# Optimization experiments

Measured on AMD Instinct MI355X. Metric: run time of the kernel, lower is better.

The kernel has to match this reference:

```python
import jax, jax.numpy as jnp
import numpy as np

B, H, W, C = 4, 64, 64, 64


def _self_atten(x, q_w, q_b, v_w, v_b, dim):
    # x: [B, N, dim]; torch Linear weight is [out, in] -> x @ W.T + b
    q = jnp.einsum('bnd,od->bno', x, q_w) + q_b
    k = q  # original module uses q_linear for both q and k
    v = jnp.einsum('bnd,od->bno', x, v_w) + v_b
    a = jax.nn.sigmoid(jnp.einsum('bnd,bmd->bnm', q, k) / jnp.sqrt(jnp.float32(dim)))
    return jnp.einsum('bnm,bmd->bnd', a, v)


def setup_inputs() -> dict:
    key = jax.random.key(0)
    ks = jax.random.split(key, 11)
    s = 0.05
    return {
        'x': jax.random.normal(ks[0], (B, H, W, C), jnp.float32),
        'hq_w': jax.random.normal(ks[1], (H, H), jnp.float32) * s,
        'hq_b': jax.random.normal(ks[2], (H,), jnp.float32) * s,
        'hv_w': jax.random.normal(ks[3], (H, H), jnp.float32) * s,
        'hv_b': jax.random.normal(ks[4], (H,), jnp.float32) * s,
        'wq_w': jax.random.normal(ks[5], (W, W), jnp.float32) * s,
        'wq_b': jax.random.normal(ks[6], (W,), jnp.float32) * s,
        'wv_w': jax.random.normal(ks[7], (W, W), jnp.float32) * s,
        'wv_b': jax.random.normal(ks[8], (W,), jnp.float32) * s,
        'h_weight': jax.random.normal(ks[9], (1,), jnp.float32) * s,
        'w_weight': jax.random.normal(ks[10], (1,), jnp.float32) * s,
    }


def reference(x, hq_w, hq_b, hv_w, hv_b, wq_w, wq_b, wv_w, wv_b, h_weight, w_weight):
    b, h, w, c = x.shape
    # height axis attention: seq = W*C, feature dim = H
    xh = jnp.transpose(x, (0, 2, 3, 1)).reshape(b, w * c, h)
    xh = _self_atten(xh, hq_w, hq_b, hv_w, hv_b, h)
    xh = jnp.transpose(xh.reshape(b, w, c, h), (0, 3, 1, 2))  # [B,H,W,C]
    x = xh * h_weight + x
    # width axis attention: seq = H*C, feature dim = W
    xw = jnp.transpose(x, (0, 1, 3, 2)).reshape(b, h * c, w)
    xw = _self_atten(xw, wq_w, wq_b, wv_w, wv_b, w)
    xw = jnp.transpose(xw.reshape(b, h, c, w), (0, 1, 3, 2))  # [B,H,W,C]
    x = xw * w_weight + x
    return x
```

## Files before the change

kernel.cpp:

```cpp
#include <hip/hip_runtime.h>
#include <hip/hip_bf16.h>


typedef __attribute__((ext_vector_type(8)))  short        short8;
typedef __attribute__((ext_vector_type(16))) float        f32x16;
typedef __attribute__((ext_vector_type(4)))  unsigned int u32x4;
typedef __attribute__((ext_vector_type(2)))  unsigned int u32x2;
typedef __attribute__((ext_vector_type(4)))  float        f32x4;

#define BHWC (4096 * 64)
#define ALPHA 0.42466089f

__device__ __forceinline__ unsigned short f2bf(float f) {
    __hip_bfloat16 h = __float2bfloat16(f);
    union { __hip_bfloat16 h; unsigned short u; } c; c.h = h;
    return c.u;
}
__device__ __forceinline__ float sigfast(float x) {
    float e, r;
    asm("v_exp_f32 %0, -%1" : "=v"(e) : "v"(x));
    e += 1.0f;
    asm("v_rcp_f32 %0, %1" : "=v"(r) : "v"(e));
    return r;
}
__device__ __forceinline__ f32x16 zero16() {
    f32x16 z;
    #pragma unroll
    for (int r = 0; r < 16; ++r) z[r] = 0.0f;
    return z;
}

template<int MODE>
__global__ __launch_bounds__(256) void proj_kernel(
    const float* __restrict__ xsrc,
    const float* __restrict__ Wq, const float* __restrict__ Bq,
    const float* __restrict__ Wv, const float* __restrict__ Bv,
    unsigned short* __restrict__ Qo, unsigned short* __restrict__ VTo)
{
    __shared__ __align__(16) unsigned short xbf[64 * 64];
    __shared__ __align__(16) unsigned short wbf[2][64 * 64];
    __shared__ __align__(16) unsigned short qst[4096];
    __shared__ __align__(16) unsigned short vst[4096];

    const int b = blockIdx.x >> 6, tile = blockIdx.x & 63, n0 = tile << 6;
    const int tid = threadIdx.x;
    const float* xb = xsrc + b * BHWC;

    for (int i = tid; i < 4096; i += 256) {
        const int d = i >> 6, nl = i & 63;
        float v;
        if (MODE == 0) v = xb[d * 4096 + n0 + nl];
        else           v = xb[tile * 4096 + i];
        xbf[nl * 64 + (d ^ ((nl & 7) << 3))] = f2bf(v);
        wbf[0][d * 64 + (nl ^ ((d & 7) << 3))] = f2bf(Wq[i] * ALPHA);
        wbf[1][d * 64 + (nl ^ ((d & 7) << 3))] = f2bf(Wv[i]);
    }
    __syncthreads();

    const int wave = tid >> 6, lane = tid & 63, l31 = lane & 31, hi = lane >> 5;
    const int mat = wave >> 1, nc = wave & 1;
    const int o = nc * 32 + l31;

    short8 bw[4];
    #pragma unroll
    for (int dc = 0; dc < 4; ++dc)
        bw[dc] = *(const short8*)&wbf[mat][o * 64 + ((dc * 16 + hi * 8) ^ ((o & 7) << 3))];

    f32x16 acc[2]; acc[0] = zero16(); acc[1] = zero16();
    #pragma unroll
    for (int dc = 0; dc < 4; ++dc) {
        #pragma unroll
        for (int mc = 0; mc < 2; ++mc) {
            const int row = mc * 32 + l31;
            const short8 a = *(const short8*)&xbf[row * 64 + ((dc * 16 + hi * 8) ^ ((row & 7) << 3))];
            acc[mc] = __builtin_amdgcn_mfma_f32_32x32x16_bf16(a, bw[dc], acc[mc], 0, 0, 0);
        }
    }
    const float bias = mat ? Bv[o] : (Bq[o] * ALPHA);

    if (mat == 0) {
        const int obase = ((o >> 4) << 9) + (((o >> 3) & 1) << 8) + (o & 7);
        #pragma unroll
        for (int mc = 0; mc < 2; ++mc)
            #pragma unroll
            for (int reg = 0; reg < 16; ++reg) {
                const int nl = (reg & 3) + 8 * (reg >> 2) + 4 * hi;
                qst[mc * 2048 + obase + nl * 8] = f2bf(acc[mc][reg] + bias);
            }
    } else {
        #pragma unroll
        for (int mc = 0; mc < 2; ++mc)
            #pragma unroll
            for (int reg = 0; reg < 16; ++reg) {
                const int nl = mc * 32 + (reg & 3) + 8 * (reg >> 2) + 4 * hi;
                vst[nc * 2048 + ((nl >> 4) << 9) + (((nl >> 3) & 1) << 8) + l31 * 8 + (nl & 7)]
                    = f2bf(acc[mc][reg] + bias);
            }
    }
    __syncthreads();

    {
        unsigned short* Qg = Qo  + b * BHWC + tile * 4096;
        unsigned short* Vg = VTo + b * BHWC + tile * 2048;
        #pragma unroll
        for (int c = tid; c < 512; c += 256)
            *(u32x4*)(Qg + c * 8) = *(const u32x4*)(qst + c * 8);
        #pragma unroll
        for (int c = tid; c < 512; c += 256) {
            const int d0 = c >> 8, r = c & 255;
            *(u32x4*)(Vg + d0 * 131072 + r * 8) = *(const u32x4*)(vst + c * 8);
        }
    }
}

template<int MODE>
__global__ __launch_bounds__(512, 4) void attn_kernel(
    const unsigned short* __restrict__ Q,
    const unsigned short* __restrict__ VT,
    const float* __restrict__ xres,
    const float* __restrict__ wsc,
    float* __restrict__ xout)
{
    __shared__ __align__(16) char smem[8 * 4608];
    float* Obuf = (float*)smem;

    const int raw = (int)blockIdx.x;
    const int L = (raw & 7) * 64 + (raw >> 3);
    const int b = L >> 7, mt = L & 127;
    const int tid = threadIdx.x, wave = tid >> 6, lane = tid & 63;
    const int l31 = lane & 31, hi = lane >> 5;
    const int kq = wave;
    const unsigned short* Qb = Q  + b * BHWC;
    const unsigned short* Vb = VT + b * BHWC;

    char* const Pw = smem + wave * 4608;
    char* const wb = Pw + l31 * 144 + 8 * hi;
    const char* const pr = Pw + l31 * 144 + 16 * hi;

    const unsigned short* qp = Qb + mt * 2048 + hi * 256 + l31 * 8;
    short8 qf[4];
    #pragma unroll
    for (int dc = 0; dc < 4; ++dc)
        qf[dc] = *(const short8*)(qp + dc * 512);

    f32x16 acc[2]; acc[0] = zero16(); acc[1] = zero16();

    auto SIGSTORE = [&](const f32x16& s, int krc) {
        #pragma unroll
        for (int q = 0; q < 4; ++q) {
            const float p0 = sigfast(s[4 * q    ]);
            const float p1 = sigfast(s[4 * q + 1]);
            const float p2 = sigfast(s[4 * q + 2]);
            const float p3 = sigfast(s[4 * q + 3]);
            u32x2 pk;
            pk[0] = (unsigned int)f2bf(p0) | ((unsigned int)f2bf(p1) << 16);
            pk[1] = (unsigned int)f2bf(p2) | ((unsigned int)f2bf(p3) << 16);
            *(u32x2*)(wb + krc * 64 + 16 * q) = pk;
        }
    };

    const unsigned short* kp = Qb + (kq * 16) * 2048 + hi * 256 + l31 * 8;
    const unsigned short* vp = Vb + (kq * 32) * 512  + hi * 256 + l31 * 8;
    short8 kfn[4];
    #pragma unroll
    for (int dc = 0; dc < 4; ++dc)
        kfn[dc] = *(const short8*)(kp + dc * 512);

    #pragma unroll 1
    for (int i = 0; i < 8; ++i) {
        short8 kf1[4];
        #pragma unroll
        for (int dc = 0; dc < 4; ++dc)
            kf1[dc] = *(const short8*)(kp + 2048 + dc * 512);

        f32x16 s = zero16();
        #pragma unroll
        for (int dc = 0; dc < 4; ++dc)
            s = __builtin_amdgcn_mfma_f32_32x32x16_bf16(kfn[dc], qf[dc], s, 0, 0, 0);
        SIGSTORE(s, 0);

        s = zero16();
        #pragma unroll
        for (int dc = 0; dc < 4; ++dc)
            s = __builtin_amdgcn_mfma_f32_32x32x16_bf16(kf1[dc], qf[dc], s, 0, 0, 0);

        short8 vf00 = *(const short8*)(vp + 0 * 512);
        short8 vf01 = *(const short8*)(vp + 0 * 512 + 131072);
        short8 vf10 = *(const short8*)(vp + 1 * 512);
        short8 vf11 = *(const short8*)(vp + 1 * 512 + 131072);

        SIGSTORE(s, 1);

        kp += 2 * 2048;
        if (i < 7) {
            #pragma unroll
            for (int dc = 0; dc < 4; ++dc)
                kfn[dc] = *(const short8*)(kp + dc * 512);
        }

        short8 pf0 = *(const short8*)(pr +  0);
        short8 pf1 = *(const short8*)(pr + 32);
        acc[0] = __builtin_amdgcn_mfma_f32_32x32x16_bf16(pf0, vf00, acc[0], 0, 0, 0);
        acc[1] = __builtin_amdgcn_mfma_f32_32x32x16_bf16(pf0, vf01, acc[1], 0, 0, 0);
        acc[0] = __builtin_amdgcn_mfma_f32_32x32x16_bf16(pf1, vf10, acc[0], 0, 0, 0);
        acc[1] = __builtin_amdgcn_mfma_f32_32x32x16_bf16(pf1, vf11, acc[1], 0, 0, 0);

        vf00 = *(const short8*)(vp + 2 * 512);
        vf01 = *(const short8*)(vp + 2 * 512 + 131072);
        vf10 = *(const short8*)(vp + 3 * 512);
        vf11 = *(const short8*)(vp + 3 * 512 + 131072);
        pf0 = *(const short8*)(pr + 64);
        pf1 = *(const short8*)(pr + 96);
        acc[0] = __builtin_amdgcn_mfma_f32_32x32x16_bf16(pf0, vf00, acc[0], 0, 0, 0);
        acc[1] = __builtin_amdgcn_mfma_f32_32x32x16_bf16(pf0, vf01, acc[1], 0, 0, 0);
        acc[0] = __builtin_amdgcn_mfma_f32_32x32x16_bf16(pf1, vf10, acc[0], 0, 0, 0);
        acc[1] = __builtin_amdgcn_mfma_f32_32x32x16_bf16(pf1, vf11, acc[1], 0, 0, 0);

        vp += 4 * 512;
    }

    __syncthreads();
    if (wave < 4) {
        float* Ob = Obuf + wave * 2112;
        #pragma unroll
        for (int dc2 = 0; dc2 < 2; ++dc2)
            #pragma unroll
            for (int reg = 0; reg < 16; ++reg)
                Ob[(dc2 * 32 + l31) * 33 + (reg & 3) + 8 * (reg >> 2) + 4 * hi] = acc[dc2][reg];
    }
    __syncthreads();
    if (wave >= 4) {
        float* Ob = Obuf + (wave - 4) * 2112;
        #pragma unroll
        for (int dc2 = 0; dc2 < 2; ++dc2)
            #pragma unroll
            for (int reg = 0; reg < 16; ++reg)
                Ob[(dc2 * 32 + l31) * 33 + (reg & 3) + 8 * (reg >> 2) + 4 * hi] += acc[dc2][reg];
    }
    __syncthreads();

    const float w = wsc[0];
    const int d = tid >> 3, ms = (tid & 7) << 2;
    long base;
    if (MODE == 0) base = (long)b * BHWC + d * 4096 + mt * 32 + ms;
    else           base = (long)b * BHWC + (mt >> 1) * 4096 + d * 64 + (mt & 1) * 32 + ms;
    const int idx = d * 33 + ms;
    const float* O0 = Obuf + 0 * 2112 + idx;
    const float* O1 = Obuf + 1 * 2112 + idx;
    const float* O2 = Obuf + 2 * 2112 + idx;
    const float* O3 = Obuf + 3 * 2112 + idx;
    f32x4 r = *(const f32x4*)(xres + base);
    f32x4 o;
    #pragma unroll
    for (int j = 0; j < 4; ++j)
        o[j] = (O0[j] + O1[j] + O2[j] + O3[j]) * w + r[j];
    *(f32x4*)(xout + base) = o;
}

extern "C" void kernel_launch(void* const* d_in, const int* in_sizes, int n_in,
                              void* d_out, int out_size, void* d_ws, size_t ws_size,
                              hipStream_t stream) {
    const float* x    = (const float*)d_in[0];
    const float* hq_w = (const float*)d_in[1];
    const float* hq_b = (const float*)d_in[2];
    const float* hv_w = (const float*)d_in[3];
    const float* hv_b = (const float*)d_in[4];
    const float* wq_w = (const float*)d_in[5];
    const float* wq_b = (const float*)d_in[6];
    const float* wv_w = (const float*)d_in[7];
    const float* wv_b = (const float*)d_in[8];
    const float* h_wt = (const float*)d_in[9];
    const float* w_wt = (const float*)d_in[10];
    float* out = (float*)d_out;

    unsigned short* Qws  = (unsigned short*)d_ws;
    unsigned short* VTws = Qws + 4 * BHWC;

    proj_kernel<0><<<256, 256, 0, stream>>>(x, hq_w, hq_b, hv_w, hv_b, Qws, VTws);
    attn_kernel<0><<<512, 512, 0, stream>>>(Qws, VTws, x, h_wt, out);
    proj_kernel<1><<<256, 256, 0, stream>>>(out, wq_w, wq_b, wv_w, wv_b, Qws, VTws);
    attn_kernel<1><<<512, 512, 0, stream>>>(Qws, VTws, out, w_wt, out);
}
```

Measured before the change: 77.24 us.

## Pre-swizzle projection weights in a prep kernel and halve projection tile size

Adds a small kernel that converts Wq (pre-scaled) and Wv to bf16 once per call, already in MFMA B-fragment order, so the projection kernels load weights straight from global instead of staging and swizzling them through LDS in every block. The projection kernel now handles 32 sequence rows per block instead of 64, which doubles the grid to 512 blocks and cuts LDS use per block. This adds two extra kernel launches and gives each wave half as many MFMAs to hide load latency behind.

New measurement: 78.12 us. Within noise of the previous version (+1.1%).

```diff
diff --git a/kernel.cpp b/kernel.cpp
--- a/kernel.cpp
+++ b/kernel.cpp
@@ -30,30 +30,45 @@
     return z;
 }
 
+__global__ __launch_bounds__(256) void wprep_kernel(
+    const float* __restrict__ Wq, const float* __restrict__ Wv,
+    unsigned short* __restrict__ wf)
+{
+    const int j = blockIdx.x * 256 + threadIdx.x;
+    const int e = j & 7;
+    int t = j >> 3;
+    const int l31 = t & 31; t >>= 5;
+    const int hi  = t & 1;  t >>= 1;
+    const int dc  = t & 3;  t >>= 2;
+    const int nc  = t & 1;  t >>= 1;
+    const int mat = t;
+    const int o = nc * 32 + l31;
+    const int d = dc * 16 + hi * 8 + e;
+    const float w = mat ? Wv[o * 64 + d] : (Wq[o * 64 + d] * ALPHA);
+    wf[j] = f2bf(w);
+}
+
 template<int MODE>
 __global__ __launch_bounds__(256) void proj_kernel(
     const float* __restrict__ xsrc,
-    const float* __restrict__ Wq, const float* __restrict__ Bq,
-    const float* __restrict__ Wv, const float* __restrict__ Bv,
+    const float* __restrict__ Bq, const float* __restrict__ Bv,
+    const unsigned short* __restrict__ wf,
     unsigned short* __restrict__ Qo, unsigned short* __restrict__ VTo)
 {
-    __shared__ __align__(16) unsigned short xbf[64 * 64];
-    __shared__ __align__(16) unsigned short wbf[2][64 * 64];
-    __shared__ __align__(16) unsigned short qst[4096];
-    __shared__ __align__(16) unsigned short vst[4096];
-
-    const int b = blockIdx.x >> 6, tile = blockIdx.x & 63, n0 = tile << 6;
+    __shared__ __align__(16) unsigned short xbf[32 * 64];
+    __shared__ __align__(16) unsigned short qst[2048];
+    __shared__ __align__(16) unsigned short vst[2048];
+
+    const int b = blockIdx.x >> 7, tile = blockIdx.x & 127, n0 = tile << 5;
     const int tid = threadIdx.x;
     const float* xb = xsrc + b * BHWC;
 
-    for (int i = tid; i < 4096; i += 256) {
-        const int d = i >> 6, nl = i & 63;
+    for (int i = tid; i < 2048; i += 256) {
+        const int d = i >> 5, nl = i & 31;
         float v;
         if (MODE == 0) v = xb[d * 4096 + n0 + nl];
-        else           v = xb[tile * 4096 + i];
+        else           v = xb[(tile >> 1) * 4096 + d * 64 + (tile & 1) * 32 + nl];
         xbf[nl * 64 + (d ^ ((nl & 7) << 3))] = f2bf(v);
-        wbf[0][d * 64 + (nl ^ ((d & 7) << 3))] = f2bf(Wq[i] * ALPHA);
-        wbf[1][d * 64 + (nl ^ ((d & 7) << 3))] = f2bf(Wv[i]);
     }
     __syncthreads();
 
@@ -61,55 +76,40 @@
     const int mat = wave >> 1, nc = wave & 1;
     const int o = nc * 32 + l31;
 
-    short8 bw[4];
-    #pragma unroll
-    for (int dc = 0; dc < 4; ++dc)
-        bw[dc] = *(const short8*)&wbf[mat][o * 64 + ((dc * 16 + hi * 8) ^ ((o & 7) << 3))];
-
-    f32x16 acc[2]; acc[0] = zero16(); acc[1] = zero16();
+    const unsigned short* wfb = wf + (mat * 2 + nc) * 2048 + hi * 256 + l31 * 8;
+    f32x16 acc = zero16();
     #pragma unroll
     for (int dc = 0; dc < 4; ++dc) {
-        #pragma unroll
-        for (int mc = 0; mc < 2; ++mc) {
-            const int row = mc * 32 + l31;
-            const short8 a = *(const short8*)&xbf[row * 64 + ((dc * 16 + hi * 8) ^ ((row & 7) << 3))];
-            acc[mc] = __builtin_amdgcn_mfma_f32_32x32x16_bf16(a, bw[dc], acc[mc], 0, 0, 0);
-        }
+        const short8 a  = *(const short8*)&xbf[l31 * 64 + ((dc * 16 + hi * 8) ^ ((l31 & 7) << 3))];
+        const short8 bw = *(const short8*)(wfb + dc * 512);
+        acc = __builtin_amdgcn_mfma_f32_32x32x16_bf16(a, bw, acc, 0, 0, 0);
     }
     const float bias = mat ? Bv[o] : (Bq[o] * ALPHA);
 
     if (mat == 0) {
         const int obase = ((o >> 4) << 9) + (((o >> 3) & 1) << 8) + (o & 7);
         #pragma unroll
-        for (int mc = 0; mc < 2; ++mc)
-            #pragma unroll
-            for (int reg = 0; reg < 16; ++reg) {
-                const int nl = (reg & 3) + 8 * (reg >> 2) + 4 * hi;
-                qst[mc * 2048 + obase + nl * 8] = f2bf(acc[mc][reg] + bias);
-            }
+        for (int reg = 0; reg < 16; ++reg) {
+            const int nl = (reg & 3) + 8 * (reg >> 2) + 4 * hi;
+            qst[obase + nl * 8] = f2bf(acc[reg] + bias);
+        }
     } else {
         #pragma unroll
-        for (int mc = 0; mc < 2; ++mc)
-            #pragma unroll
-            for (int reg = 0; reg < 16; ++reg) {
-                const int nl = mc * 32 + (reg & 3) + 8 * (reg >> 2) + 4 * hi;
-                vst[nc * 2048 + ((nl >> 4) << 9) + (((nl >> 3) & 1) << 8) + l31 * 8 + (nl & 7)]
-                    = f2bf(acc[mc][reg] + bias);
-            }
+        for (int reg = 0; reg < 16; ++reg) {
+            const int nl = (reg & 3) + 8 * (reg >> 2) + 4 * hi;
+            vst[nc * 1024 + ((nl >> 4) << 9) + (((nl >> 3) & 1) << 8) + l31 * 8 + (nl & 7)]
+                = f2bf(acc[reg] + bias);
+        }
     }
     __syncthreads();
 
     {
-        unsigned short* Qg = Qo  + b * BHWC + tile * 4096;
-        unsigned short* Vg = VTo + b * BHWC + tile * 2048;
-        #pragma unroll
-        for (int c = tid; c < 512; c += 256)
-            *(u32x4*)(Qg + c * 8) = *(const u32x4*)(qst + c * 8);
-        #pragma unroll
-        for (int c = tid; c < 512; c += 256) {
-            const int d0 = c >> 8, r = c & 255;
-            *(u32x4*)(Vg + d0 * 131072 + r * 8) = *(const u32x4*)(vst + c * 8);
-        }
+        unsigned short* Qg = Qo  + b * BHWC + tile * 2048;
+        unsigned short* Vg = VTo + b * BHWC + tile * 1024;
+        const int c = tid;
+        *(u32x4*)(Qg + c * 8) = *(const u32x4*)(qst + c * 8);
+        const int d0 = c >> 7, r = c & 127;
+        *(u32x4*)(Vg + d0 * 131072 + r * 8) = *(const u32x4*)(vst + c * 8);
     }
 }
 
@@ -275,9 +275,13 @@
 
     unsigned short* Qws  = (unsigned short*)d_ws;
     unsigned short* VTws = Qws + 4 * BHWC;
-
-    proj_kernel<0><<<256, 256, 0, stream>>>(x, hq_w, hq_b, hv_w, hv_b, Qws, VTws);
+    unsigned short* wf1  = VTws + 4 * BHWC;
+    unsigned short* wf2  = wf1 + 8192;
+
+    wprep_kernel<<<32, 256, 0, stream>>>(hq_w, hv_w, wf1);
+    wprep_kernel<<<32, 256, 0, stream>>>(wq_w, wv_w, wf2);
+    proj_kernel<0><<<512, 256, 0, stream>>>(x, hq_b, hv_b, wf1, Qws, VTws);
     attn_kernel<0><<<512, 512, 0, stream>>>(Qws, VTws, x, h_wt, out);
-    proj_kernel<1><<<256, 256, 0, stream>>>(out, wq_w, wq_b, wv_w, wv_b, Qws, VTws);
+    proj_kernel<1><<<512, 256, 0, stream>>>(out, wq_b, wv_b, wf2, Qws, VTws);
     attn_kernel<1><<<512, 512, 0, stream>>>(Qws, VTws, out, w_wt, out);
 }
```
